# Kernel optimization log

Hardware: AMD Instinct MI355X
Metric: run time of the kernel (lower is better)

The kernel has to match this reference:

```python
import jax, jax.numpy as jnp
import numpy as np

D_MODEL = 1024
NUM_HEADS = 16
D_K = D_MODEL // NUM_HEADS
B, S = 2, 2048


def setup_inputs() -> dict:
    key = jax.random.key(0)
    ks = jax.random.split(key, 11)
    scale = 1.0 / np.sqrt(D_MODEL)
    inp = {
        "Q": jax.random.normal(ks[0], (B, S, D_MODEL), jnp.float32),
        "K": jax.random.normal(ks[1], (B, S, D_MODEL), jnp.float32),
        "V": jax.random.normal(ks[2], (B, S, D_MODEL), jnp.float32),
        "mask": jnp.tril(jnp.ones((S, S), jnp.int32))[None, None, :, :],  # causal [1,1,S,S]
        "Wq": jax.random.normal(ks[3], (D_MODEL, D_MODEL), jnp.float32) * scale,
        "bq": jax.random.normal(ks[4], (D_MODEL,), jnp.float32) * scale,
        "Wk": jax.random.normal(ks[5], (D_MODEL, D_MODEL), jnp.float32) * scale,
        "bk": jax.random.normal(ks[6], (D_MODEL,), jnp.float32) * scale,
        "Wv": jax.random.normal(ks[7], (D_MODEL, D_MODEL), jnp.float32) * scale,
        "bv": jax.random.normal(ks[8], (D_MODEL,), jnp.float32) * scale,
        "Wo": jax.random.normal(ks[9], (D_MODEL, D_MODEL), jnp.float32) * scale,
        "bo": jax.random.normal(ks[10], (D_MODEL,), jnp.float32) * scale,
    }
    return inp


def _split_heads(x):
    b, s, _ = x.shape
    return x.reshape(b, s, NUM_HEADS, D_K).transpose(0, 2, 1, 3)  # [B,H,S,d_k]


def reference(Q, K, V, mask, Wq, bq, Wk, bk, Wv, bv, Wo, bo):
    q = _split_heads(Q @ Wq.T + bq)
    k = _split_heads(K @ Wk.T + bk)
    v = _split_heads(V @ Wv.T + bv)
    scores = jnp.einsum("bhqd,bhkd->bhqk", q, k) / jnp.sqrt(jnp.float32(D_K))
    scores = jnp.where(mask == 0, jnp.float32(-1e9), scores)
    probs = jax.nn.softmax(scores, axis=-1)
    attn = jnp.einsum("bhqk,bhkd->bhqd", probs, v)  # [B,H,S,d_k]
    attn = attn.transpose(0, 2, 1, 3).reshape(Q.shape[0], Q.shape[1], D_MODEL)
    return attn @ Wo.T + bo
```

## Files before the change

kernel.cpp:

```cpp
#include <hip/hip_runtime.h>
#include <hip/hip_bf16.h>

typedef __attribute__((ext_vector_type(8))) short short8;
typedef __attribute__((ext_vector_type(4))) short short4v;
typedef __attribute__((ext_vector_type(4))) float f32x4;

static __device__ __forceinline__ short f2bf(float f) {
    __hip_bfloat16 h = __float2bfloat16(f);
    return __builtin_bit_cast(short, h);
}

#define GLOAD16(g, l) __builtin_amdgcn_global_load_lds( \
    (const __attribute__((address_space(1))) void*)(g), \
    (__attribute__((address_space(3))) void*)(l), 16, 0, 0)

__global__ __launch_bounds__(256) void convert_qkv(
        const float* __restrict__ a, const float* __restrict__ b, const float* __restrict__ c,
        short* __restrict__ oa, short* __restrict__ ob, short* __restrict__ oc, int n4) {
    const float* in = blockIdx.y == 0 ? a : blockIdx.y == 1 ? b : c;
    short* out = blockIdx.y == 0 ? oa : blockIdx.y == 1 ? ob : oc;
    int i = blockIdx.x * blockDim.x + threadIdx.x;
    int stride = gridDim.x * blockDim.x;
    for (; i < n4; i += stride) {
        f32x4 v = reinterpret_cast<const f32x4*>(in)[i];
        short4v o;
        o.x = f2bf(v.x); o.y = f2bf(v.y); o.z = f2bf(v.z); o.w = f2bf(v.w);
        reinterpret_cast<short4v*>(out)[i] = o;
    }
}

__global__ __launch_bounds__(256) void convert_w(
        const float* __restrict__ a, const float* __restrict__ b,
        const float* __restrict__ c, const float* __restrict__ d,
        short* __restrict__ oa, short* __restrict__ ob,
        short* __restrict__ oc, short* __restrict__ od, int n4) {
    const float* in = blockIdx.y == 0 ? a : blockIdx.y == 1 ? b : blockIdx.y == 2 ? c : d;
    short* out = blockIdx.y == 0 ? oa : blockIdx.y == 1 ? ob : blockIdx.y == 2 ? oc : od;
    int i = blockIdx.x * blockDim.x + threadIdx.x;
    int stride = gridDim.x * blockDim.x;
    for (; i < n4; i += stride) {
        f32x4 v = reinterpret_cast<const f32x4*>(in)[i];
        short4v o;
        o.x = f2bf(v.x); o.y = f2bf(v.y); o.z = f2bf(v.z); o.w = f2bf(v.w);
        reinterpret_cast<short4v*>(out)[i] = o;
    }
}

__device__ __forceinline__ void gemm_kloop(
        const short* __restrict__ Abase, const short* __restrict__ Wbase,
        short* aSb, short* bSb, f32x4 (&acc)[4][2], int w, int lane) {
    const int lr = lane >> 3;
    const int lcs = ((lane & 7) ^ lr) * 8;
    const int l15 = lane & 15, lq = lane >> 4;
    const int wr = w >> 1, wc = w & 1;
    const int cA0 = ((0 + lq) ^ (l15 & 7)) * 8;
    const int cA1 = ((4 + lq) ^ (l15 & 7)) * 8;

#pragma unroll
    for (int j = 0; j < 4; ++j) {
        int r0 = w * 32 + j * 8;
        GLOAD16(&Abase[(size_t)(r0 + lr) * 1024 + lcs], &aSb[r0 * 64]);
    }
#pragma unroll
    for (int j = 0; j < 2; ++j) {
        int r0 = w * 16 + j * 8;
        GLOAD16(&Wbase[(size_t)(r0 + lr) * 1024 + lcs], &bSb[r0 * 64]);
    }

    for (int t = 0; t < 16; ++t) {
        const int cur = t & 1;
        if (t < 15) {
            const int k0 = (t + 1) * 64;
            const int nb = cur ^ 1;
#pragma unroll
            for (int j = 0; j < 4; ++j) {
                int r0 = w * 32 + j * 8;
                GLOAD16(&Abase[(size_t)(r0 + lr) * 1024 + k0 + lcs], &aSb[nb * 8192 + r0 * 64]);
            }
#pragma unroll
            for (int j = 0; j < 2; ++j) {
                int r0 = w * 16 + j * 8;
                GLOAD16(&Wbase[(size_t)(r0 + lr) * 1024 + k0 + lcs], &bSb[nb * 4096 + r0 * 64]);
            }
            asm volatile("s_waitcnt vmcnt(6)" ::: "memory");
        } else {
            asm volatile("s_waitcnt vmcnt(0)" ::: "memory");
        }
        __builtin_amdgcn_s_barrier();
        __builtin_amdgcn_sched_barrier(0);
#pragma unroll
        for (int kf = 0; kf < 2; ++kf) {
            const int ck = kf ? cA1 : cA0;
            short8 af[4], bfr[2];
#pragma unroll
            for (int mi = 0; mi < 4; ++mi)
                af[mi] = *reinterpret_cast<const short8*>(
                    &aSb[cur * 8192 + (wr * 64 + mi * 16 + l15) * 64 + ck]);
#pragma unroll
            for (int ni = 0; ni < 2; ++ni)
                bfr[ni] = *reinterpret_cast<const short8*>(
                    &bSb[cur * 4096 + (wc * 32 + ni * 16 + l15) * 64 + ck]);
#pragma unroll
            for (int mi = 0; mi < 4; ++mi)
#pragma unroll
                for (int ni = 0; ni < 2; ++ni)
                    acc[mi][ni] = __builtin_amdgcn_mfma_f32_16x16x32_bf16(
                        af[mi], bfr[ni], acc[mi][ni], 0, 0, 0);
        }
        asm volatile("s_waitcnt lgkmcnt(0)" ::: "memory");
        __builtin_amdgcn_sched_barrier(0);
        __builtin_amdgcn_s_barrier();
    }
}

__global__ __launch_bounds__(256, 3) void gemm_qkv(
        const short* __restrict__ Qb, const short* __restrict__ Kb, const short* __restrict__ Vb,
        const short* __restrict__ Wq, const short* __restrict__ Wk, const short* __restrict__ Wv,
        const float* __restrict__ bq, const float* __restrict__ bk, const float* __restrict__ bv,
        short* __restrict__ q_, short* __restrict__ k_, short* __restrict__ vT) {
    __shared__ __align__(16) short aSb[2 * 128 * 64];
    __shared__ __align__(16) short bSb[2 * 64 * 64];
    const int tid = threadIdx.x;
    const int lane = tid & 63;
    const int w = tid >> 6;
    const int y = blockIdx.y;
    const int wg = (blockIdx.x & 7) * 64 + (blockIdx.x >> 3);
    const int bn = wg & 15;
    const int bm = wg >> 4;
    const int l15 = lane & 15, lq = lane >> 4;
    const int wr = w >> 1, wc = w & 1;

    const short* A = y == 0 ? Qb : y == 1 ? Kb : Vb;
    const short* W = y == 0 ? Wq : y == 1 ? Wk : Wv;
    const float* bias = y == 0 ? bq : y == 1 ? bk : bv;

    f32x4 acc[4][2] = {};
    gemm_kloop(&A[(size_t)(bm * 128) * 1024], &W[(size_t)(bn * 64) * 1024],
               aSb, bSb, acc, w, lane);

#pragma unroll
    for (int mi = 0; mi < 4; ++mi) {
#pragma unroll
        for (int ni = 0; ni < 2; ++ni) {
#pragma unroll
            for (int i = 0; i < 4; ++i) {
                int m = bm * 128 + wr * 64 + mi * 16 + lq * 4 + i;
                int n = bn * 64 + wc * 32 + ni * 16 + l15;
                float v = acc[mi][ni][i] + bias[n];
                int b = m >> 11, s = m & 2047, h = n >> 6, d = n & 63;
                if (y == 0) {
                    q_[((size_t)(b * 16 + h) * 2048 + s) * 64 + d] = f2bf(v * 0.125f);
                } else if (y == 1) {
                    k_[((size_t)(b * 16 + h) * 2048 + s) * 64 + d] = f2bf(v);
                } else {
                    vT[((size_t)(b * 16 + h) * 64 + d) * 2048 + s] = f2bf(v);
                }
            }
        }
    }
}

__global__ __launch_bounds__(256, 3) void gemm_o(
        const short* __restrict__ A, const short* __restrict__ W,
        const float* __restrict__ bias, float* __restrict__ out) {
    __shared__ __align__(16) short aSb[2 * 128 * 64];
    __shared__ __align__(16) short bSb[2 * 64 * 64];
    const int tid = threadIdx.x;
    const int lane = tid & 63;
    const int w = tid >> 6;
    const int wg = (blockIdx.x & 7) * 64 + (blockIdx.x >> 3);
    const int bn = wg & 15;
    const int bm = wg >> 4;
    const int l15 = lane & 15, lq = lane >> 4;
    const int wr = w >> 1, wc = w & 1;

    f32x4 acc[4][2] = {};
    gemm_kloop(&A[(size_t)(bm * 128) * 1024], &W[(size_t)(bn * 64) * 1024],
               aSb, bSb, acc, w, lane);

#pragma unroll
    for (int mi = 0; mi < 4; ++mi)
#pragma unroll
        for (int ni = 0; ni < 2; ++ni)
#pragma unroll
            for (int i = 0; i < 4; ++i) {
                int m = bm * 128 + wr * 64 + mi * 16 + lq * 4 + i;
                int n = bn * 64 + wc * 32 + ni * 16 + l15;
                out[(size_t)m * 1024 + n] = acc[mi][ni][i] + bias[n];
            }
}

__global__ __launch_bounds__(512, 4) void attn_fwd(
        const short* __restrict__ qh, const short* __restrict__ kh,
        const short* __restrict__ vT, short* __restrict__ attn) {
    __shared__ __align__(16) short kS[2][64 * 72];
    __shared__ __align__(16) short vS[2][64 * 72];
    __shared__ __align__(16) short pS[8][16 * 72];
    const int tid = threadIdx.x;
    const int lane = tid & 63;
    const int w = tid >> 6;
    const int l15 = lane & 15, lq = lane >> 4;
    const int bh = blockIdx.x & 31;
    const int qt = 15 - (blockIdx.x >> 5);
    const int b = bh >> 4, h = bh & 15;
    const size_t head = (size_t)bh * 2048 * 64;
    const short* qp = qh + head;
    const short* kp = kh + head;
    const short* vp = vT + head;

    const int qw0 = qt * 128 + w * 16;

    short8 qf_[2];
#pragma unroll
    for (int kf = 0; kf < 2; ++kf)
        qf_[kf] = *reinterpret_cast<const short8*>(
            &qp[(size_t)(qw0 + l15) * 64 + kf * 32 + lq * 8]);

    f32x4 o[4] = {};
    float m_[4], l_[4];
#pragma unroll
    for (int i = 0; i < 4; ++i) { m_[i] = -1e30f; l_[i] = 0.f; }

    const int sr = tid >> 3;
    const int sc = (tid & 7) * 8;

    const int nt = 2 * qt + 2;
    short8 kreg = *reinterpret_cast<const short8*>(&kp[(size_t)sr * 64 + sc]);
    short8 vreg = *reinterpret_cast<const short8*>(&vp[(size_t)sr * 2048 + sc]);
    *reinterpret_cast<short8*>(&kS[0][sr * 72 + sc]) = kreg;
    *reinterpret_cast<short8*>(&vS[0][sr * 72 + sc]) = vreg;
    __syncthreads();

    for (int t = 0; t < nt; ++t) {
        const int p = t & 1;
        if (t + 1 < nt) {
            kreg = *reinterpret_cast<const short8*>(
                &kp[(size_t)((t + 1) * 64 + sr) * 64 + sc]);
            vreg = *reinterpret_cast<const short8*>(
                &vp[(size_t)sr * 2048 + (t + 1) * 64 + sc]);
        }
        if (t * 64 <= qw0 + 15) {
            f32x4 s[4] = {};
#pragma unroll
            for (int kf = 0; kf < 2; ++kf) {
                short8 bfr[4];
#pragma unroll
                for (int cf = 0; cf < 4; ++cf)
                    bfr[cf] = *reinterpret_cast<const short8*>(
                        &kS[p][(cf * 16 + l15) * 72 + kf * 32 + lq * 8]);
#pragma unroll
                for (int cf = 0; cf < 4; ++cf)
                    s[cf] = __builtin_amdgcn_mfma_f32_16x16x32_bf16(
                        qf_[kf], bfr[cf], s[cf], 0, 0, 0);
            }
            if (t * 64 + 63 > qw0) {
#pragma unroll
                for (int cf = 0; cf < 4; ++cf)
#pragma unroll
                    for (int i = 0; i < 4; ++i) {
                        int qg = qw0 + lq * 4 + i;
                        int kg = t * 64 + cf * 16 + l15;
                        if (kg > qg) s[cf][i] = -1e30f;
                    }
            }
            float mx[4], scale[4];
#pragma unroll
            for (int i = 0; i < 4; ++i) {
                float v = fmaxf(fmaxf(s[0][i], s[1][i]), fmaxf(s[2][i], s[3][i]));
#pragma unroll
                for (int x = 1; x < 16; x <<= 1) v = fmaxf(v, __shfl_xor(v, x));
                float mn = fmaxf(m_[i], v);
                scale[i] = __expf(m_[i] - mn);
                m_[i] = mn;
                mx[i] = mn;
            }
            float rs[4] = {0.f, 0.f, 0.f, 0.f};
#pragma unroll
            for (int cf = 0; cf < 4; ++cf) {
#pragma unroll
                for (int i = 0; i < 4; ++i) {
                    float pv = __expf(s[cf][i] - mx[i]);
                    rs[i] += pv;
                    pS[w][(lq * 4 + i) * 72 + cf * 16 + l15] = f2bf(pv);
                }
            }
#pragma unroll
            for (int i = 0; i < 4; ++i) {
                float r = rs[i];
#pragma unroll
                for (int x = 1; x < 16; x <<= 1) r += __shfl_xor(r, x);
                l_[i] = l_[i] * scale[i] + r;
            }
#pragma unroll
            for (int df = 0; df < 4; ++df)
#pragma unroll
                for (int i = 0; i < 4; ++i)
                    o[df][i] *= scale[i];
            asm volatile("s_waitcnt lgkmcnt(0)" ::: "memory");
            __builtin_amdgcn_sched_barrier(0);
#pragma unroll
            for (int kk = 0; kk < 2; ++kk) {
                short8 pa, vb[4];
                pa = *reinterpret_cast<const short8*>(
                    &pS[w][l15 * 72 + kk * 32 + lq * 8]);
#pragma unroll
                for (int df = 0; df < 4; ++df)
                    vb[df] = *reinterpret_cast<const short8*>(
                        &vS[p][(df * 16 + l15) * 72 + kk * 32 + lq * 8]);
#pragma unroll
                for (int df = 0; df < 4; ++df)
                    o[df] = __builtin_amdgcn_mfma_f32_16x16x32_bf16(
                        pa, vb[df], o[df], 0, 0, 0);
            }
        }
        if (t + 1 < nt) {
            *reinterpret_cast<short8*>(&kS[p ^ 1][sr * 72 + sc]) = kreg;
            *reinterpret_cast<short8*>(&vS[p ^ 1][sr * 72 + sc]) = vreg;
        }
        __syncthreads();
    }

#pragma unroll
    for (int i = 0; i < 4; ++i) {
        float rinv = 1.0f / l_[i];
        int sg = qw0 + lq * 4 + i;
        size_t mrow = (size_t)b * 2048 + sg;
#pragma unroll
        for (int df = 0; df < 4; ++df) {
            int col = h * 64 + df * 16 + l15;
            attn[mrow * 1024 + col] = f2bf(o[df][i] * rinv);
        }
    }
}

extern "C" void kernel_launch(void* const* d_in, const int* in_sizes, int n_in,
                              void* d_out, int out_size, void* d_ws, size_t ws_size,
                              hipStream_t stream) {
    const float* Q  = (const float*)d_in[0];
    const float* K  = (const float*)d_in[1];
    const float* V  = (const float*)d_in[2];
    const float* Wq = (const float*)d_in[4];
    const float* bq = (const float*)d_in[5];
    const float* Wk = (const float*)d_in[6];
    const float* bk = (const float*)d_in[7];
    const float* Wv = (const float*)d_in[8];
    const float* bv = (const float*)d_in[9];
    const float* Wo = (const float*)d_in[10];
    const float* bo = (const float*)d_in[11];

    char* ws = (char*)d_ws;
    short* Qb   = (short*)(ws);
    short* Kb   = (short*)(ws + 8388608);
    short* Vb   = (short*)(ws + 16777216);
    short* Wqb  = (short*)(ws + 25165824);
    short* Wkb  = (short*)(ws + 27262976);
    short* Wvb  = (short*)(ws + 29360128);
    short* Wob  = (short*)(ws + 31457280);
    short* q_   = (short*)(ws + 33554432);
    short* k_   = (short*)(ws + 41943040);
    short* vT   = (short*)(ws + 50331648);
    short* attn = Qb;

    dim3 cb(256);
    convert_qkv<<<dim3(1024, 3), cb, 0, stream>>>(Q, K, V, Qb, Kb, Vb, 4194304 / 4);
    convert_w<<<dim3(512, 4), cb, 0, stream>>>(Wq, Wk, Wv, Wo, Wqb, Wkb, Wvb, Wob, 1048576 / 4);

    gemm_qkv<<<dim3(512, 3), cb, 0, stream>>>(Qb, Kb, Vb, Wqb, Wkb, Wvb,
                                              bq, bk, bv, q_, k_, vT);

    attn_fwd<<<dim3(512), dim3(512), 0, stream>>>(q_, k_, vT, attn);

    gemm_o<<<dim3(512), cb, 0, stream>>>(attn, Wob, bo, (float*)d_out);
}
```

Before: 263.7 us.

## Retile QKV GEMM to 128x128 and restructure attention with transposed scores

The QKV projection now uses 128x128 output tiles with a single-buffered K loop. This replaces the 128x64 double-buffered shared kloop to raise arithmetic intensity per block. The attention kernel moves to 64-query blocks of 4 waves and computes S transposed so each lane owns one query row. It uses exp2 with a log2e-prescaled Q, lazy rescaling of the running max (threshold 8), packed bf16 conversion and single-buffered K/V tiles. Dropping double buffering and adding an extra barrier may expose load latency, and the lazy rescale trades precision headroom for fewer rescale operations.

```diff
diff --git a/kernel.cpp b/kernel.cpp
--- a/kernel.cpp
+++ b/kernel.cpp
@@ -8,6 +8,18 @@
 static __device__ __forceinline__ short f2bf(float f) {
     __hip_bfloat16 h = __float2bfloat16(f);
     return __builtin_bit_cast(short, h);
+}
+
+static __device__ __forceinline__ float exp2fast(float x) {
+    float r;
+    asm("v_exp_f32 %0, %1" : "=v"(r) : "v"(x));
+    return r;
+}
+
+static __device__ __forceinline__ unsigned cvt_pk_bf16(float a, float b) {
+    unsigned r;
+    asm("v_cvt_pk_bf16_f32 %0, %1, %2" : "=v"(r) : "v"(a), "v"(b));
+    return r;
 }
 
 #define GLOAD16(g, l) __builtin_amdgcn_global_load_lds( \
@@ -46,6 +58,94 @@
     }
 }
 
+__global__ __launch_bounds__(256, 3) void gemm_qkv(
+        const short* __restrict__ Qb, const short* __restrict__ Kb, const short* __restrict__ Vb,
+        const short* __restrict__ Wq, const short* __restrict__ Wk, const short* __restrict__ Wv,
+        const float* __restrict__ bq, const float* __restrict__ bk, const float* __restrict__ bv,
+        short* __restrict__ q_, short* __restrict__ k_, short* __restrict__ vT) {
+    __shared__ __align__(16) short aS[128 * 64];
+    __shared__ __align__(16) short bS[128 * 64];
+    const int tid = threadIdx.x;
+    const int lane = tid & 63;
+    const int w = tid >> 6;
+    const int wr = w >> 1, wc = w & 1;
+    const int l15 = lane & 15, lq = lane >> 4;
+    const int lr = lane >> 3;
+    const int lcs = ((lane & 7) ^ lr) * 8;
+    const int y = blockIdx.y;
+    const int wg = (blockIdx.x & 7) * 32 + (blockIdx.x >> 3);
+    const int bn = wg & 7;
+    const int bm = wg >> 3;
+
+    const short* A = y == 0 ? Qb : y == 1 ? Kb : Vb;
+    const short* W = y == 0 ? Wq : y == 1 ? Wk : Wv;
+    const float* bias = y == 0 ? bq : y == 1 ? bk : bv;
+    const short* Ab = A + (size_t)(bm * 128) * 1024;
+    const short* Wb = W + (size_t)(bn * 128) * 1024;
+
+    f32x4 acc[4][4] = {};
+
+    for (int t = 0; t < 16; ++t) {
+        const int k0 = t * 64;
+#pragma unroll
+        for (int j = 0; j < 4; ++j) {
+            int r0 = w * 32 + j * 8;
+            GLOAD16(&Ab[(size_t)(r0 + lr) * 1024 + k0 + lcs], &aS[r0 * 64]);
+        }
+#pragma unroll
+        for (int j = 0; j < 4; ++j) {
+            int r0 = w * 32 + j * 8;
+            GLOAD16(&Wb[(size_t)(r0 + lr) * 1024 + k0 + lcs], &bS[r0 * 64]);
+        }
+        asm volatile("s_waitcnt vmcnt(0)" ::: "memory");
+        __builtin_amdgcn_s_barrier();
+#pragma unroll
+        for (int kf = 0; kf < 2; ++kf) {
+            const int ck = ((kf * 4 + lq) ^ (l15 & 7)) * 8;
+            short8 af[4], bfr[4];
+#pragma unroll
+            for (int mi = 0; mi < 4; ++mi)
+                af[mi] = *reinterpret_cast<const short8*>(
+                    &aS[(wr * 64 + mi * 16 + l15) * 64 + ck]);
+#pragma unroll
+            for (int ni = 0; ni < 4; ++ni)
+                bfr[ni] = *reinterpret_cast<const short8*>(
+                    &bS[(wc * 64 + ni * 16 + l15) * 64 + ck]);
+#pragma unroll
+            for (int mi = 0; mi < 4; ++mi)
+#pragma unroll
+                for (int ni = 0; ni < 4; ++ni)
+                    acc[mi][ni] = __builtin_amdgcn_mfma_f32_16x16x32_bf16(
+                        af[mi], bfr[ni], acc[mi][ni], 0, 0, 0);
+        }
+        asm volatile("s_waitcnt lgkmcnt(0)" ::: "memory");
+        __builtin_amdgcn_sched_barrier(0);
+        __builtin_amdgcn_s_barrier();
+    }
+
+    const float QSCALE = 0.125f * 1.44269504f;
+#pragma unroll
+    for (int mi = 0; mi < 4; ++mi) {
+#pragma unroll
+        for (int ni = 0; ni < 4; ++ni) {
+#pragma unroll
+            for (int i = 0; i < 4; ++i) {
+                int m = bm * 128 + wr * 64 + mi * 16 + lq * 4 + i;
+                int n = bn * 128 + wc * 64 + ni * 16 + l15;
+                float v = acc[mi][ni][i] + bias[n];
+                int b = m >> 11, s = m & 2047, h = n >> 6, d = n & 63;
+                if (y == 0) {
+                    q_[((size_t)(b * 16 + h) * 2048 + s) * 64 + d] = f2bf(v * QSCALE);
+                } else if (y == 1) {
+                    k_[((size_t)(b * 16 + h) * 2048 + s) * 64 + d] = f2bf(v);
+                } else {
+                    vT[((size_t)(b * 16 + h) * 64 + d) * 2048 + s] = f2bf(v);
+                }
+            }
+        }
+    }
+}
+
 __device__ __forceinline__ void gemm_kloop(
         const short* __restrict__ Abase, const short* __restrict__ Wbase,
         short* aSb, short* bSb, f32x4 (&acc)[4][2], int w, int lane) {
@@ -110,53 +210,6 @@
         asm volatile("s_waitcnt lgkmcnt(0)" ::: "memory");
         __builtin_amdgcn_sched_barrier(0);
         __builtin_amdgcn_s_barrier();
-    }
-}
-
-__global__ __launch_bounds__(256, 3) void gemm_qkv(
-        const short* __restrict__ Qb, const short* __restrict__ Kb, const short* __restrict__ Vb,
-        const short* __restrict__ Wq, const short* __restrict__ Wk, const short* __restrict__ Wv,
-        const float* __restrict__ bq, const float* __restrict__ bk, const float* __restrict__ bv,
-        short* __restrict__ q_, short* __restrict__ k_, short* __restrict__ vT) {
-    __shared__ __align__(16) short aSb[2 * 128 * 64];
-    __shared__ __align__(16) short bSb[2 * 64 * 64];
-    const int tid = threadIdx.x;
-    const int lane = tid & 63;
-    const int w = tid >> 6;
-    const int y = blockIdx.y;
-    const int wg = (blockIdx.x & 7) * 64 + (blockIdx.x >> 3);
-    const int bn = wg & 15;
-    const int bm = wg >> 4;
-    const int l15 = lane & 15, lq = lane >> 4;
-    const int wr = w >> 1, wc = w & 1;
-
-    const short* A = y == 0 ? Qb : y == 1 ? Kb : Vb;
-    const short* W = y == 0 ? Wq : y == 1 ? Wk : Wv;
-    const float* bias = y == 0 ? bq : y == 1 ? bk : bv;
-
-    f32x4 acc[4][2] = {};
-    gemm_kloop(&A[(size_t)(bm * 128) * 1024], &W[(size_t)(bn * 64) * 1024],
-               aSb, bSb, acc, w, lane);
-
-#pragma unroll
-    for (int mi = 0; mi < 4; ++mi) {
-#pragma unroll
-        for (int ni = 0; ni < 2; ++ni) {
-#pragma unroll
-            for (int i = 0; i < 4; ++i) {
-                int m = bm * 128 + wr * 64 + mi * 16 + lq * 4 + i;
-                int n = bn * 64 + wc * 32 + ni * 16 + l15;
-                float v = acc[mi][ni][i] + bias[n];
-                int b = m >> 11, s = m & 2047, h = n >> 6, d = n & 63;
-                if (y == 0) {
-                    q_[((size_t)(b * 16 + h) * 2048 + s) * 64 + d] = f2bf(v * 0.125f);
-                } else if (y == 1) {
-                    k_[((size_t)(b * 16 + h) * 2048 + s) * 64 + d] = f2bf(v);
-                } else {
-                    vT[((size_t)(b * 16 + h) * 64 + d) * 2048 + s] = f2bf(v);
-                }
-            }
-        }
     }
 }
 
@@ -190,25 +243,24 @@
             }
 }
 
-__global__ __launch_bounds__(512, 4) void attn_fwd(
+__global__ __launch_bounds__(256, 4) void attn_fwd(
         const short* __restrict__ qh, const short* __restrict__ kh,
         const short* __restrict__ vT, short* __restrict__ attn) {
-    __shared__ __align__(16) short kS[2][64 * 72];
-    __shared__ __align__(16) short vS[2][64 * 72];
-    __shared__ __align__(16) short pS[8][16 * 72];
+    __shared__ __align__(16) short kS[64 * 72];
+    __shared__ __align__(16) short vS[64 * 72];
+    __shared__ __align__(16) int pS[4][16 * 36];
     const int tid = threadIdx.x;
     const int lane = tid & 63;
     const int w = tid >> 6;
     const int l15 = lane & 15, lq = lane >> 4;
     const int bh = blockIdx.x & 31;
-    const int qt = 15 - (blockIdx.x >> 5);
+    const int qt = 31 - (blockIdx.x >> 5);
     const int b = bh >> 4, h = bh & 15;
     const size_t head = (size_t)bh * 2048 * 64;
     const short* qp = qh + head;
     const short* kp = kh + head;
     const short* vp = vT + head;
-
-    const int qw0 = qt * 128 + w * 16;
+    const int qw0 = qt * 64 + w * 16;
 
     short8 qf_[2];
 #pragma unroll
@@ -217,112 +269,118 @@
             &qp[(size_t)(qw0 + l15) * 64 + kf * 32 + lq * 8]);
 
     f32x4 o[4] = {};
-    float m_[4], l_[4];
-#pragma unroll
-    for (int i = 0; i < 4; ++i) { m_[i] = -1e30f; l_[i] = 0.f; }
+    float m_ = -1e30f, l_ = 0.f;
 
     const int sr = tid >> 3;
     const int sc = (tid & 7) * 8;
 
-    const int nt = 2 * qt + 2;
-    short8 kreg = *reinterpret_cast<const short8*>(&kp[(size_t)sr * 64 + sc]);
-    short8 vreg = *reinterpret_cast<const short8*>(&vp[(size_t)sr * 2048 + sc]);
-    *reinterpret_cast<short8*>(&kS[0][sr * 72 + sc]) = kreg;
-    *reinterpret_cast<short8*>(&vS[0][sr * 72 + sc]) = vreg;
+    const int nt = qt + 1;
+    short8 kra = *reinterpret_cast<const short8*>(&kp[(size_t)sr * 64 + sc]);
+    short8 krb = *reinterpret_cast<const short8*>(&kp[(size_t)(sr + 32) * 64 + sc]);
+    short8 vra = *reinterpret_cast<const short8*>(&vp[(size_t)sr * 2048 + sc]);
+    short8 vrb = *reinterpret_cast<const short8*>(&vp[(size_t)(sr + 32) * 2048 + sc]);
+    *reinterpret_cast<short8*>(&kS[sr * 72 + sc]) = kra;
+    *reinterpret_cast<short8*>(&kS[(sr + 32) * 72 + sc]) = krb;
+    *reinterpret_cast<short8*>(&vS[sr * 72 + sc]) = vra;
+    *reinterpret_cast<short8*>(&vS[(sr + 32) * 72 + sc]) = vrb;
     __syncthreads();
 
     for (int t = 0; t < nt; ++t) {
-        const int p = t & 1;
         if (t + 1 < nt) {
-            kreg = *reinterpret_cast<const short8*>(
+            kra = *reinterpret_cast<const short8*>(
                 &kp[(size_t)((t + 1) * 64 + sr) * 64 + sc]);
-            vreg = *reinterpret_cast<const short8*>(
+            krb = *reinterpret_cast<const short8*>(
+                &kp[(size_t)((t + 1) * 64 + sr + 32) * 64 + sc]);
+            vra = *reinterpret_cast<const short8*>(
                 &vp[(size_t)sr * 2048 + (t + 1) * 64 + sc]);
-        }
-        if (t * 64 <= qw0 + 15) {
-            f32x4 s[4] = {};
-#pragma unroll
-            for (int kf = 0; kf < 2; ++kf) {
-                short8 bfr[4];
-#pragma unroll
-                for (int cf = 0; cf < 4; ++cf)
-                    bfr[cf] = *reinterpret_cast<const short8*>(
-                        &kS[p][(cf * 16 + l15) * 72 + kf * 32 + lq * 8]);
-#pragma unroll
-                for (int cf = 0; cf < 4; ++cf)
-                    s[cf] = __builtin_amdgcn_mfma_f32_16x16x32_bf16(
-                        qf_[kf], bfr[cf], s[cf], 0, 0, 0);
+            vrb = *reinterpret_cast<const short8*>(
+                &vp[(size_t)(sr + 32) * 2048 + (t + 1) * 64 + sc]);
+        }
+        f32x4 s[4] = {};
+#pragma unroll
+        for (int kf = 0; kf < 2; ++kf) {
+            short8 kfr[4];
+#pragma unroll
+            for (int cf = 0; cf < 4; ++cf)
+                kfr[cf] = *reinterpret_cast<const short8*>(
+                    &kS[(cf * 16 + l15) * 72 + kf * 32 + lq * 8]);
+#pragma unroll
+            for (int cf = 0; cf < 4; ++cf)
+                s[cf] = __builtin_amdgcn_mfma_f32_16x16x32_bf16(
+                    kfr[cf], qf_[kf], s[cf], 0, 0, 0);
+        }
+        if (t == qt) {
+            const int q = qw0 + l15;
+#pragma unroll
+            for (int cf = 0; cf < 4; ++cf)
+#pragma unroll
+                for (int i = 0; i < 4; ++i)
+                    if (t * 64 + cf * 16 + lq * 4 + i > q) s[cf][i] = -1e30f;
+        }
+        float pmax = fmaxf(fmaxf(fmaxf(s[0][0], s[0][1]), fmaxf(s[0][2], s[0][3])),
+                           fmaxf(fmaxf(s[1][0], s[1][1]), fmaxf(s[1][2], s[1][3])));
+        pmax = fmaxf(pmax, fmaxf(fmaxf(fmaxf(s[2][0], s[2][1]), fmaxf(s[2][2], s[2][3])),
+                                 fmaxf(fmaxf(s[3][0], s[3][1]), fmaxf(s[3][2], s[3][3]))));
+        pmax = fmaxf(pmax, __shfl_xor(pmax, 16));
+        pmax = fmaxf(pmax, __shfl_xor(pmax, 32));
+        if (!__all(pmax - m_ <= 8.0f)) {
+            float mnew = fmaxf(m_, pmax);
+            float scl = exp2fast(m_ - mnew);
+            m_ = mnew;
+            l_ *= scl;
+            float s0 = __shfl(scl, lq * 4 + 0);
+            float s1 = __shfl(scl, lq * 4 + 1);
+            float s2 = __shfl(scl, lq * 4 + 2);
+            float s3 = __shfl(scl, lq * 4 + 3);
+#pragma unroll
+            for (int df = 0; df < 4; ++df) {
+                o[df][0] *= s0; o[df][1] *= s1; o[df][2] *= s2; o[df][3] *= s3;
             }
-            if (t * 64 + 63 > qw0) {
-#pragma unroll
-                for (int cf = 0; cf < 4; ++cf)
-#pragma unroll
-                    for (int i = 0; i < 4; ++i) {
-                        int qg = qw0 + lq * 4 + i;
-                        int kg = t * 64 + cf * 16 + l15;
-                        if (kg > qg) s[cf][i] = -1e30f;
-                    }
-            }
-            float mx[4], scale[4];
-#pragma unroll
-            for (int i = 0; i < 4; ++i) {
-                float v = fmaxf(fmaxf(s[0][i], s[1][i]), fmaxf(s[2][i], s[3][i]));
-#pragma unroll
-                for (int x = 1; x < 16; x <<= 1) v = fmaxf(v, __shfl_xor(v, x));
-                float mn = fmaxf(m_[i], v);
-                scale[i] = __expf(m_[i] - mn);
-                m_[i] = mn;
-                mx[i] = mn;
-            }
-            float rs[4] = {0.f, 0.f, 0.f, 0.f};
-#pragma unroll
-            for (int cf = 0; cf < 4; ++cf) {
-#pragma unroll
-                for (int i = 0; i < 4; ++i) {
-                    float pv = __expf(s[cf][i] - mx[i]);
-                    rs[i] += pv;
-                    pS[w][(lq * 4 + i) * 72 + cf * 16 + l15] = f2bf(pv);
-                }
-            }
-#pragma unroll
-            for (int i = 0; i < 4; ++i) {
-                float r = rs[i];
-#pragma unroll
-                for (int x = 1; x < 16; x <<= 1) r += __shfl_xor(r, x);
-                l_[i] = l_[i] * scale[i] + r;
-            }
+        }
+        float rsum = 0.f;
+#pragma unroll
+        for (int cf = 0; cf < 4; ++cf) {
+            float p0 = exp2fast(s[cf][0] - m_);
+            float p1 = exp2fast(s[cf][1] - m_);
+            float p2 = exp2fast(s[cf][2] - m_);
+            float p3 = exp2fast(s[cf][3] - m_);
+            rsum += (p0 + p1) + (p2 + p3);
+            pS[w][l15 * 36 + cf * 8 + lq * 2 + 0] = cvt_pk_bf16(p0, p1);
+            pS[w][l15 * 36 + cf * 8 + lq * 2 + 1] = cvt_pk_bf16(p2, p3);
+        }
+        rsum += __shfl_xor(rsum, 16);
+        rsum += __shfl_xor(rsum, 32);
+        l_ += rsum;
+        asm volatile("s_waitcnt lgkmcnt(0)" ::: "memory");
+        __builtin_amdgcn_sched_barrier(0);
+#pragma unroll
+        for (int kk = 0; kk < 2; ++kk) {
+            short8 pa = *reinterpret_cast<const short8*>(
+                &pS[w][l15 * 36 + kk * 16 + lq * 4]);
+            short8 vb[4];
 #pragma unroll
             for (int df = 0; df < 4; ++df)
-#pragma unroll
-                for (int i = 0; i < 4; ++i)
-                    o[df][i] *= scale[i];
-            asm volatile("s_waitcnt lgkmcnt(0)" ::: "memory");
-            __builtin_amdgcn_sched_barrier(0);
-#pragma unroll
-            for (int kk = 0; kk < 2; ++kk) {
-                short8 pa, vb[4];
-                pa = *reinterpret_cast<const short8*>(
-                    &pS[w][l15 * 72 + kk * 32 + lq * 8]);
-#pragma unroll
-                for (int df = 0; df < 4; ++df)
-                    vb[df] = *reinterpret_cast<const short8*>(
-                        &vS[p][(df * 16 + l15) * 72 + kk * 32 + lq * 8]);
-#pragma unroll
-                for (int df = 0; df < 4; ++df)
-                    o[df] = __builtin_amdgcn_mfma_f32_16x16x32_bf16(
-                        pa, vb[df], o[df], 0, 0, 0);
-            }
-        }
+                vb[df] = *reinterpret_cast<const short8*>(
+                    &vS[(df * 16 + l15) * 72 + kk * 32 + lq * 8]);
+#pragma unroll
+            for (int df = 0; df < 4; ++df)
+                o[df] = __builtin_amdgcn_mfma_f32_16x16x32_bf16(
+                    pa, vb[df], o[df], 0, 0, 0);
+        }
+        __syncthreads();
         if (t + 1 < nt) {
-            *reinterpret_cast<short8*>(&kS[p ^ 1][sr * 72 + sc]) = kreg;
-            *reinterpret_cast<short8*>(&vS[p ^ 1][sr * 72 + sc]) = vreg;
+            *reinterpret_cast<short8*>(&kS[sr * 72 + sc]) = kra;
+            *reinterpret_cast<short8*>(&kS[(sr + 32) * 72 + sc]) = krb;
+            *reinterpret_cast<short8*>(&vS[sr * 72 + sc]) = vra;
+            *reinterpret_cast<short8*>(&vS[(sr + 32) * 72 + sc]) = vrb;
         }
         __syncthreads();
     }
 
 #pragma unroll
     for (int i = 0; i < 4; ++i) {
-        float rinv = 1.0f / l_[i];
+        float li = __shfl(l_, lq * 4 + i);
+        float rinv = 1.0f / li;
         int sg = qw0 + lq * 4 + i;
         size_t mrow = (size_t)b * 2048 + sg;
 #pragma unroll
@@ -365,10 +423,10 @@
     convert_qkv<<<dim3(1024, 3), cb, 0, stream>>>(Q, K, V, Qb, Kb, Vb, 4194304 / 4);
     convert_w<<<dim3(512, 4), cb, 0, stream>>>(Wq, Wk, Wv, Wo, Wqb, Wkb, Wvb, Wob, 1048576 / 4);
 
-    gemm_qkv<<<dim3(512, 3), cb, 0, stream>>>(Qb, Kb, Vb, Wqb, Wkb, Wvb,
+    gemm_qkv<<<dim3(256, 3), cb, 0, stream>>>(Qb, Kb, Vb, Wqb, Wkb, Wvb,
                                               bq, bk, bv, q_, k_, vT);
 
-    attn_fwd<<<dim3(512), dim3(512), 0, stream>>>(q_, k_, vT, attn);
+    attn_fwd<<<dim3(1024), cb, 0, stream>>>(q_, k_, vT, attn);
 
     gemm_o<<<dim3(512), cb, 0, stream>>>(attn, Wob, bo, (float*)d_out);
 }
```

Result: faster. 227.9 us (-13.6%).
